# Kernel tuning notes

Measured on AMD Instinct MI355X. Metric: run time of the kernel, lower is better.

## Reference

```python
import jax, jax.numpy as jnp
import numpy as np

LOSS_EPS = 1e-6  # module eps, used to clamp IoU before log
DEN_EPS = 1e-10  # parallel-edge guard in segment intersection
IN_TOL = 1e-5    # tolerance for point-in-box containment test


def _corners(boxes):
    # boxes: (n,5) = (x, y, w, h, angle) -> (n,4,2) corner coords
    x, y, w, h, a = (boxes[:, i] for i in range(5))
    c, s = jnp.cos(a)[:, None], jnp.sin(a)[:, None]
    dx = (w * 0.5)[:, None] * jnp.array([-1.0, 1.0, 1.0, -1.0], boxes.dtype)
    dy = (h * 0.5)[:, None] * jnp.array([-1.0, -1.0, 1.0, 1.0], boxes.dtype)
    px = x[:, None] + dx * c - dy * s
    py = y[:, None] + dx * s + dy * c
    return jnp.stack([px, py], axis=-1)


def _cross(u, v):
    return u[..., 0] * v[..., 1] - u[..., 1] * v[..., 0]


def _in_box(pts, boxes):
    # pts: (n,4,2) corners of the *other* box; boxes: (n,5). Rotate into box frame.
    a = boxes[:, 4]
    c, s = jnp.cos(a)[:, None], jnp.sin(a)[:, None]
    d = pts - boxes[:, None, 0:2]
    lx = d[..., 0] * c + d[..., 1] * s
    ly = -d[..., 0] * s + d[..., 1] * c
    return (jnp.abs(lx) <= boxes[:, None, 2] * 0.5 + IN_TOL) & \
           (jnp.abs(ly) <= boxes[:, None, 3] * 0.5 + IN_TOL)


def box_iou_rotated(pred, target):
    # Differentiable rotated-box IoU via convex polygon intersection.
    n = pred.shape[0]
    c1 = _corners(pred)    # (n,4,2)
    c2 = _corners(target)  # (n,4,2)

    # --- all 4x4 edge-pair segment intersections ---
    p1, p2 = c1, jnp.roll(c1, -1, axis=1)
    q1, q2 = c2, jnp.roll(c2, -1, axis=1)
    r = (p2 - p1)[:, :, None, :]            # (n,4,1,2)
    s = (q2 - q1)[:, None, :, :]            # (n,1,4,2)
    qp = q1[:, None, :, :] - p1[:, :, None, :]
    den = _cross(r, s)                      # (n,4,4)
    den_ok = jnp.abs(den) > DEN_EPS
    den_safe = jnp.where(den_ok, den, 1.0)
    t = _cross(qp, s) / den_safe
    u = _cross(qp, r) / den_safe
    ok = den_ok & (t >= 0) & (t <= 1) & (u >= 0) & (u <= 1)
    t_safe = jnp.where(ok, t, 0.0)
    ipts = p1[:, :, None, :] + t_safe[..., None] * r  # (n,4,4,2)

    # --- candidate vertex set: 16 edge intersections + contained corners ---
    pts = jnp.concatenate([ipts.reshape(n, 16, 2), c1, c2], axis=1)      # (n,24,2)
    mask = jnp.concatenate([ok.reshape(n, 16), _in_box(c1, target), _in_box(c2, pred)], axis=1)

    num = mask.sum(axis=1)  # int
    numf = jnp.maximum(num, 1).astype(pts.dtype)
    cen = (pts * mask[..., None]).sum(axis=1) / numf[:, None]  # centroid of valid pts

    # sort valid points CCW around centroid; invalid points pushed to the end
    d = pts - cen[:, None, :]
    ang = jnp.where(mask, jnp.arctan2(d[..., 1], d[..., 0]), 1e8)
    order = jnp.argsort(ang, axis=1)
    spts = jnp.take_along_axis(pts, order[..., None], axis=1)
    smask = jnp.take_along_axis(mask, order, axis=1)
    # replace trailing invalid slots with the first (valid) vertex -> zero shoelace terms
    spts = jnp.where(smask[..., None], spts, spts[:, :1, :])

    area_i = 0.5 * jnp.abs(_cross(spts, jnp.roll(spts, -1, axis=1)).sum(axis=1))
    area_i = jnp.where(num >= 3, area_i, 0.0)

    a1 = pred[:, 2] * pred[:, 3]
    a2 = target[:, 2] * target[:, 3]
    return area_i / jnp.maximum(a1 + a2 - area_i, DEN_EPS)


def setup_inputs() -> dict:
    key = jax.random.key(0)
    ks = jax.random.split(key, 6)
    n = 500000
    ctr = jax.random.uniform(ks[0], (n, 2), minval=0.0, maxval=1024.0)
    wh = jax.random.uniform(ks[1], (n, 2), minval=8.0, maxval=128.0)
    ang = jax.random.uniform(ks[2], (n, 1), minval=-np.pi, maxval=np.pi)
    pred = jnp.concatenate([ctr, wh, ang], axis=1).astype(jnp.float32)
    ctr2 = ctr + 4.0 * jax.random.normal(ks[3], (n, 2))
    wh2 = wh * jax.random.uniform(ks[4], (n, 2), minval=0.85, maxval=1.2)
    ang2 = ang + 0.1 * jax.random.normal(ks[5], (n, 1))
    target = jnp.concatenate([ctr2, wh2, ang2], axis=1).astype(jnp.float32)
    return {"pred": pred, "target": target}


def reference(pred, target):
    # RotatedIoULoss.forward: weight=None, linear=False, reduction='mean', loss_weight=1.0
    ious = jnp.clip(box_iou_rotated(pred, target), LOSS_EPS, None)
    loss = -jnp.log(ious)
    return 1.0 * loss.mean()
```

## Files before the change

kernel.cpp:

```cpp
#include <hip/hip_runtime.h>
#include <math.h>

#define DEN_EPS_F 1e-10f

__device__ __forceinline__ void axclip(float p, float d, float h,
                                       float& t0, float& t1) {
    float dc = (fabsf(d) < 1e-12f) ? 1e-12f : d;
    float rd = __builtin_amdgcn_rcpf(dc);
    float ta = (-h - p) * rd;
    float tb = ( h - p) * rd;
    t0 = fmaxf(t0, fminf(ta, tb));
    t1 = fminf(t1, fmaxf(ta, tb));
}

__device__ __forceinline__ float box_pair_loss(const float* bp, const float* bt) {
    float x1 = bp[0], y1 = bp[1], w1 = bp[2], h1 = bp[3], a1 = bp[4];
    float x2 = bt[0], y2 = bt[1], w2 = bt[2], h2 = bt[3], a2 = bt[4];
    float s1, c1, s2, c2;
    __sincosf(a1, &s1, &c1);
    __sincosf(a2, &s2, &c2);

    float hw1 = 0.5f * w1, hh1 = 0.5f * h1;
    float hw2 = 0.5f * w2, hh2 = 0.5f * h2;

    float tx = x2 - x1, ty = y2 - y1;

    float ux1 = hw1 * c1, uy1 = hw1 * s1;
    float vx1 = -hh1 * s1, vy1 = hh1 * c1;
    float ux2 = hw2 * c2, uy2 = hw2 * s2;
    float vx2 = -hh2 * s2, vy2 = hh2 * c2;

    float px[4], py[4], qx[4], qy[4];
    px[0] = -ux1 - vx1; py[0] = -uy1 - vy1;
    px[1] =  ux1 - vx1; py[1] =  uy1 - vy1;
    px[2] =  ux1 + vx1; py[2] =  uy1 + vy1;
    px[3] = -ux1 + vx1; py[3] = -uy1 + vy1;
    qx[0] = tx - ux2 - vx2; qy[0] = ty - uy2 - vy2;
    qx[1] = tx + ux2 - vx2; qy[1] = ty + uy2 - vy2;
    qx[2] = tx + ux2 + vx2; qy[2] = ty + uy2 + vy2;
    qx[3] = tx - ux2 + vx2; qy[3] = ty - uy2 + vy2;

    float plx[4], ply[4], qlx[4], qly[4];
#pragma unroll
    for (int k = 0; k < 4; ++k) {
        float dx = px[k] - tx, dy = py[k] - ty;
        plx[k] = dx * c2 + dy * s2;
        ply[k] = -dx * s2 + dy * c2;
        float ex = qx[k], ey = qy[k];
        qlx[k] = ex * c1 + ey * s1;
        qly[k] = -ex * s1 + ey * c1;
    }

    float acc = 0.0f;
#pragma unroll
    for (int k = 0; k < 4; ++k) {
        int k1 = (k + 1) & 3;
        float dxl = plx[k1] - plx[k], dyl = ply[k1] - ply[k];
        float t0 = 0.0f, t1 = 1.0f;
        axclip(plx[k], dxl, hw2, t0, t1);
        axclip(ply[k], dyl, hh2, t0, t1);
        bool valid = t1 > t0;
        float rx = px[k1] - px[k], ry = py[k1] - py[k];
        float Ax = fmaf(t0, rx, px[k]), Ay = fmaf(t0, ry, py[k]);
        float Bx = fmaf(t1, rx, px[k]), By = fmaf(t1, ry, py[k]);
        float cr = Ax * By - Ay * Bx;
        acc += valid ? cr : 0.0f;
    }
#pragma unroll
    for (int k = 0; k < 4; ++k) {
        int k1 = (k + 1) & 3;
        float dxl = qlx[k1] - qlx[k], dyl = qly[k1] - qly[k];
        float t0 = 0.0f, t1 = 1.0f;
        axclip(qlx[k], dxl, hw1, t0, t1);
        axclip(qly[k], dyl, hh1, t0, t1);
        bool valid = t1 > t0;
        float rx = qx[k1] - qx[k], ry = qy[k1] - qy[k];
        float Ax = fmaf(t0, rx, qx[k]), Ay = fmaf(t0, ry, qy[k]);
        float Bx = fmaf(t1, rx, qx[k]), By = fmaf(t1, ry, qy[k]);
        float cr = Ax * By - Ay * Bx;
        acc += valid ? cr : 0.0f;
    }

    float area = 0.5f * fabsf(acc);
    float uni = fmaxf(fmaf(w1, h1, w2 * h2) - area, DEN_EPS_F);
    float iou = area * __builtin_amdgcn_rcpf(uni);
    return -__logf(fmaxf(iou, 1e-6f));
}

#define BOX_PER_THREAD 4

__global__ __launch_bounds__(256, 2) void riou_loss_kernel(
        const float* __restrict__ pred, const float* __restrict__ target,
        float* __restrict__ out, int n, float inv_n) {
    int t = blockIdx.x * blockDim.x + threadIdx.x;
    int base = t * BOX_PER_THREAD;
    float loss = 0.0f;

    if (base + BOX_PER_THREAD - 1 < n) {
        const float4* p4 = reinterpret_cast<const float4*>(pred) + (size_t)t * 5;
        const float4* t4 = reinterpret_cast<const float4*>(target) + (size_t)t * 5;
        float fp[20], ft[20];
#pragma unroll
        for (int k = 0; k < 5; ++k) {
            float4 v = p4[k];
            fp[4 * k + 0] = v.x; fp[4 * k + 1] = v.y;
            fp[4 * k + 2] = v.z; fp[4 * k + 3] = v.w;
            float4 u = t4[k];
            ft[4 * k + 0] = u.x; ft[4 * k + 1] = u.y;
            ft[4 * k + 2] = u.z; ft[4 * k + 3] = u.w;
        }
#pragma unroll
        for (int b = 0; b < BOX_PER_THREAD; ++b)
            loss += box_pair_loss(fp + 5 * b, ft + 5 * b);
    } else if (base < n) {
        for (int b = 0; b < BOX_PER_THREAD; ++b) {
            int idx = base + b;
            if (idx < n)
                loss += box_pair_loss(pred + (size_t)idx * 5,
                                      target + (size_t)idx * 5);
        }
    }

#pragma unroll
    for (int off = 32; off > 0; off >>= 1)
        loss += __shfl_down(loss, off, 64);

    __shared__ float wsum[4];
    int lane = threadIdx.x & 63;
    int wid = threadIdx.x >> 6;
    if (lane == 0) wsum[wid] = loss;
    __syncthreads();
    if (threadIdx.x == 0) {
        float s = (wsum[0] + wsum[1]) + (wsum[2] + wsum[3]);
        atomicAdd(out, s * inv_n);
    }
}

extern "C" void kernel_launch(void* const* d_in, const int* in_sizes, int n_in,
                              void* d_out, int out_size, void* d_ws, size_t ws_size,
                              hipStream_t stream) {
    const float* pred = (const float*)d_in[0];
    const float* target = (const float*)d_in[1];
    float* out = (float*)d_out;
    int n = in_sizes[0] / 5;

    hipMemsetAsync(out, 0, sizeof(float), stream);

    int threads_needed = (n + BOX_PER_THREAD - 1) / BOX_PER_THREAD;
    int block = 256;
    int grid = (threads_needed + block - 1) / block;
    riou_loss_kernel<<<grid, block, 0, stream>>>(pred, target, out, n,
                                                 1.0f / (float)n);
}
```

Measured before the change: 75.98 us.

## Reformulate clipped-edge area algebraically in relative frames; use single-wave blocks

```diff
diff --git a/kernel.cpp b/kernel.cpp
--- a/kernel.cpp
+++ b/kernel.cpp
@@ -3,93 +3,84 @@
 
 #define DEN_EPS_F 1e-10f
 
-__device__ __forceinline__ void axclip(float p, float d, float h,
-                                       float& t0, float& t1) {
+__device__ __forceinline__ float safe_rcp(float d) {
     float dc = (fabsf(d) < 1e-12f) ? 1e-12f : d;
-    float rd = __builtin_amdgcn_rcpf(dc);
-    float ta = (-h - p) * rd;
-    float tb = ( h - p) * rd;
-    t0 = fmaxf(t0, fminf(ta, tb));
-    t1 = fminf(t1, fmaxf(ta, tb));
+    return __builtin_amdgcn_rcpf(dc);
+}
+
+__device__ __forceinline__ float clip_dt(float px_, float py_,
+                                         float rdx, float rdy,
+                                         float hx, float hy) {
+    float tax = (-hx - px_) * rdx, tbx = (hx - px_) * rdx;
+    float tay = (-hy - py_) * rdy, tby = (hy - py_) * rdy;
+    float lox = fminf(tax, tbx), hix = fmaxf(tax, tbx);
+    float loy = fminf(tay, tby), hiy = fmaxf(tay, tby);
+    float t0 = fmaxf(fmaxf(lox, loy), 0.0f);
+    float t1 = fminf(fminf(hix, hiy), 1.0f);
+    return fmaxf(t1 - t0, 0.0f);
 }
 
 __device__ __forceinline__ float box_pair_loss(const float* bp, const float* bt) {
-    float x1 = bp[0], y1 = bp[1], w1 = bp[2], h1 = bp[3], a1 = bp[4];
-    float x2 = bt[0], y2 = bt[1], w2 = bt[2], h2 = bt[3], a2 = bt[4];
-    float s1, c1, s2, c2;
-    __sincosf(a1, &s1, &c1);
-    __sincosf(a2, &s2, &c2);
+    float x1 = bp[0], y1 = bp[1], w1 = bp[2], h1 = bp[3], ang1 = bp[4];
+    float x2 = bt[0], y2 = bt[1], w2 = bt[2], h2 = bt[3], ang2 = bt[4];
+    float s1, c1, sd, cd;
+    __sincosf(ang1, &s1, &c1);
+    __sincosf(ang2 - ang1, &sd, &cd);
 
     float hw1 = 0.5f * w1, hh1 = 0.5f * h1;
     float hw2 = 0.5f * w2, hh2 = 0.5f * h2;
 
     float tx = x2 - x1, ty = y2 - y1;
+    float cx = tx * c1 + ty * s1;
+    float cy = -tx * s1 + ty * c1;
 
-    float ux1 = hw1 * c1, uy1 = hw1 * s1;
-    float vx1 = -hh1 * s1, vy1 = hh1 * c1;
-    float ux2 = hw2 * c2, uy2 = hw2 * s2;
-    float vx2 = -hh2 * s2, vy2 = hh2 * c2;
+    float ux = hw2 * cd, uy = hw2 * sd;
+    float vx = -hh2 * sd, vy = hh2 * cd;
 
-    float px[4], py[4], qx[4], qy[4];
-    px[0] = -ux1 - vx1; py[0] = -uy1 - vy1;
-    px[1] =  ux1 - vx1; py[1] =  uy1 - vy1;
-    px[2] =  ux1 + vx1; py[2] =  uy1 + vy1;
-    px[3] = -ux1 + vx1; py[3] = -uy1 + vy1;
-    qx[0] = tx - ux2 - vx2; qy[0] = ty - uy2 - vy2;
-    qx[1] = tx + ux2 - vx2; qy[1] = ty + uy2 - vy2;
-    qx[2] = tx + ux2 + vx2; qy[2] = ty + uy2 + vy2;
-    qx[3] = tx - ux2 + vx2; qy[3] = ty - uy2 + vy2;
+    float e0x = cx - ux, e1x = cx + ux;
+    float qx0 = e0x - vx, qx1 = e1x - vx, qx2 = e1x + vx, qx3 = e0x + vx;
+    float e0y = cy - uy, e1y = cy + uy;
+    float qy0 = e0y - vy, qy1 = e1y - vy, qy2 = e1y + vy, qy3 = e0y + vy;
 
-    float plx[4], ply[4], qlx[4], qly[4];
-#pragma unroll
-    for (int k = 0; k < 4; ++k) {
-        float dx = px[k] - tx, dy = py[k] - ty;
-        plx[k] = dx * c2 + dy * s2;
-        ply[k] = -dx * s2 + dy * c2;
-        float ex = qx[k], ey = qy[k];
-        qlx[k] = ex * c1 + ey * s1;
-        qly[k] = -ex * s1 + ey * c1;
-    }
+    float Axx = hw1 * cd, Axy = -hw1 * sd;
+    float Bxx = hh1 * sd, Byy = hh1 * cd;
+    float gx = cx * cd + cy * sd;
+    float gy = -cx * sd + cy * cd;
+    float f0x = -Axx - gx, f1x = Axx - gx;
+    float px0 = f0x - Bxx, px1 = f1x - Bxx, px2 = f1x + Bxx, px3 = f0x + Bxx;
+    float f0y = -Axy - gy, f1y = Axy - gy;
+    float py0 = f0y - Byy, py1 = f1y - Byy, py2 = f1y + Byy, py3 = f0y + Byy;
 
-    float acc = 0.0f;
-#pragma unroll
-    for (int k = 0; k < 4; ++k) {
-        int k1 = (k + 1) & 3;
-        float dxl = plx[k1] - plx[k], dyl = ply[k1] - ply[k];
-        float t0 = 0.0f, t1 = 1.0f;
-        axclip(plx[k], dxl, hw2, t0, t1);
-        axclip(ply[k], dyl, hh2, t0, t1);
-        bool valid = t1 > t0;
-        float rx = px[k1] - px[k], ry = py[k1] - py[k];
-        float Ax = fmaf(t0, rx, px[k]), Ay = fmaf(t0, ry, py[k]);
-        float Bx = fmaf(t1, rx, px[k]), By = fmaf(t1, ry, py[k]);
-        float cr = Ax * By - Ay * Bx;
-        acc += valid ? cr : 0.0f;
-    }
-#pragma unroll
-    for (int k = 0; k < 4; ++k) {
-        int k1 = (k + 1) & 3;
-        float dxl = qlx[k1] - qlx[k], dyl = qly[k1] - qly[k];
-        float t0 = 0.0f, t1 = 1.0f;
-        axclip(qlx[k], dxl, hw1, t0, t1);
-        axclip(qly[k], dyl, hh1, t0, t1);
-        bool valid = t1 > t0;
-        float rx = qx[k1] - qx[k], ry = qy[k1] - qy[k];
-        float Ax = fmaf(t0, rx, qx[k]), Ay = fmaf(t0, ry, qy[k]);
-        float Bx = fmaf(t1, rx, qx[k]), By = fmaf(t1, ry, qy[k]);
-        float cr = Ax * By - Ay * Bx;
-        acc += valid ? cr : 0.0f;
-    }
+    float rAx = 0.5f * safe_rcp(Axx), rAy = 0.5f * safe_rcp(Axy);
+    float rBx = 0.5f * safe_rcp(Bxx), rBy = 0.5f * safe_rcp(Byy);
+    float dtP = clip_dt(px0, py0, rAx, rAy, hw2, hh2)
+              + clip_dt(px1, py1, rBx, rBy, hw2, hh2)
+              + clip_dt(px2, py2, -rAx, -rAy, hw2, hh2)
+              + clip_dt(px3, py3, -rBx, -rBy, hw2, hh2);
 
+    float rux = 0.5f * safe_rcp(ux), ruy = 0.5f * safe_rcp(uy);
+    float rvx = 0.5f * safe_rcp(vx), rvy = 0.5f * safe_rcp(vy);
+    float dq0 = clip_dt(qx0, qy0, rux, ruy, hw1, hh1);
+    float dq1 = clip_dt(qx1, qy1, rvx, rvy, hw1, hh1);
+    float dq2 = clip_dt(qx2, qy2, -rux, -ruy, hw1, hh1);
+    float dq3 = clip_dt(qx3, qy3, -rvx, -rvy, hw1, hh1);
+    float dtQ = (dq0 + dq2) + (dq1 + dq3);
+
+    float Ku = 2.0f * (cx * uy - cy * ux);
+    float Kv = 2.0f * (cx * vy - cy * vx);
+    float A1 = w1 * h1, A2 = w2 * h2;
+    float acc = 0.5f * (A1 * dtP + A2 * dtQ)
+              + Ku * (dq0 - dq2) + Kv * (dq1 - dq3);
     float area = 0.5f * fabsf(acc);
-    float uni = fmaxf(fmaf(w1, h1, w2 * h2) - area, DEN_EPS_F);
+
+    float uni = fmaxf((A1 + A2) - area, DEN_EPS_F);
     float iou = area * __builtin_amdgcn_rcpf(uni);
     return -__logf(fmaxf(iou, 1e-6f));
 }
 
 #define BOX_PER_THREAD 4
 
-__global__ __launch_bounds__(256, 2) void riou_loss_kernel(
+__global__ __launch_bounds__(64, 4) void riou_loss_kernel(
         const float* __restrict__ pred, const float* __restrict__ target,
         float* __restrict__ out, int n, float inv_n) {
     int t = blockIdx.x * blockDim.x + threadIdx.x;
@@ -124,16 +115,8 @@
 #pragma unroll
     for (int off = 32; off > 0; off >>= 1)
         loss += __shfl_down(loss, off, 64);
-
-    __shared__ float wsum[4];
-    int lane = threadIdx.x & 63;
-    int wid = threadIdx.x >> 6;
-    if (lane == 0) wsum[wid] = loss;
-    __syncthreads();
-    if (threadIdx.x == 0) {
-        float s = (wsum[0] + wsum[1]) + (wsum[2] + wsum[3]);
-        atomicAdd(out, s * inv_n);
-    }
+    if (threadIdx.x == 0)
+        atomicAdd(out, loss * inv_n);
 }
 
 extern "C" void kernel_launch(void* const* d_in, const int* in_sizes, int n_in,
@@ -147,7 +130,7 @@
     hipMemsetAsync(out, 0, sizeof(float), stream);
 
     int threads_needed = (n + BOX_PER_THREAD - 1) / BOX_PER_THREAD;
-    int block = 256;
+    int block = 64;
     int grid = (threads_needed + block - 1) / block;
     riou_loss_kernel<<<grid, block, 0, stream>>>(pred, target, out, n,
                                                  1.0f / (float)n);
```

Result: slower. 93.83 us (+23.5%).
